# Optimization experiments

Measured on AMD Instinct MI355X. Metric: run time of the kernel, lower is better.

The kernel has to match this reference:

```python
import jax, jax.numpy as jnp
import numpy as np

N_NODES = 100000
N_EDGES = 1600000
IN_FEAT = 256
HIDDEN = 64
N_CLASSES = 16


def gcn_conv(x, edge_index, W, b):
    """PyG GCNConv: add self-loops, symmetric normalization, linear+aggregate."""
    n = x.shape[0]
    src, dst = edge_index[0], edge_index[1]
    loops = jnp.arange(n, dtype=src.dtype)
    src = jnp.concatenate([src, loops])
    dst = jnp.concatenate([dst, loops])
    # in-degree on graph with self-loops
    deg = jax.ops.segment_sum(jnp.ones(src.shape[0], dtype=x.dtype), dst, num_segments=n)
    dinv = jnp.where(deg > 0, jax.lax.rsqrt(deg), 0.0)
    h = x @ W                                  # [N, out]
    norm = dinv[src] * dinv[dst]               # [E+N]
    msg = h[src] * norm[:, None]                # gather + scale (memory-bound)
    out = jax.ops.segment_sum(msg, dst, num_segments=n)  # scatter-add
    return out + b


def setup_inputs() -> dict:
    key = jax.random.key(0)
    ks = jax.random.split(key, 5)
    x = jax.random.normal(ks[0], (N_NODES, IN_FEAT), dtype=jnp.float32)
    edge_index = jax.random.randint(ks[1], (2, N_EDGES), 0, N_NODES, dtype=jnp.int64)
    W1 = jax.random.normal(ks[2], (IN_FEAT, HIDDEN), dtype=jnp.float32) * (1.0 / np.sqrt(IN_FEAT))
    b1 = jnp.zeros((HIDDEN,), dtype=jnp.float32)
    W2 = jax.random.normal(ks[3], (HIDDEN, N_CLASSES), dtype=jnp.float32) * (1.0 / np.sqrt(HIDDEN))
    b2 = jnp.zeros((N_CLASSES,), dtype=jnp.float32)
    return {"x": x, "edge_index": edge_index, "W1": W1, "b1": b1, "W2": W2, "b2": b2}


def reference(x, edge_index, W1, b1, W2, b2):
    h = gcn_conv(x, edge_index, W1, b1)
    h = jax.nn.relu(h)
    # dropout p=0.5 is identity in eval mode (training=False)
    out = gcn_conv(h, edge_index, W2, b2)
    return out
```

## Files before the change

### kernel.cpp

```cpp
#include <hip/hip_runtime.h>

#define NN 100000
#define NE 1600000
#define FIN 256
#define FH 64
#define FC 16

#define SCAN_CHUNK 1024
#define NB_SCAN ((NN + SCAN_CHUNK - 1) / SCAN_CHUNK)
#define NB_COUNT ((NE + 255) / 256)
#define NB_GEMM1 ((NN + 63) / 64)
#define NB_FUSED (5 * NB_GEMM1)

typedef int v2i __attribute__((ext_vector_type(2)));

__device__ __forceinline__ float4 fma4(float4 v, float w, float4 a) {
    a.x = fmaf(v.x, w, a.x); a.y = fmaf(v.y, w, a.y);
    a.z = fmaf(v.z, w, a.z); a.w = fmaf(v.w, w, a.w);
    return a;
}
__device__ __forceinline__ float4 add4(float4 a, float4 v) {
    a.x += v.x; a.y += v.y; a.z += v.z; a.w += v.w;
    return a;
}
__device__ __forceinline__ float4 xor_add4(float4 r, int m) {
    r.x += __shfl_xor(r.x, m, 64); r.y += __shfl_xor(r.y, m, 64);
    r.z += __shfl_xor(r.z, m, 64); r.w += __shfl_xor(r.w, m, 64);
    return r;
}

__global__ void detect_k(const int* __restrict__ ei, int* __restrict__ flag) {
    if (threadIdx.x == 0 && blockIdx.x == 0) {
        int z = (ei[1] == 0) & (ei[3] == 0) & (ei[5] == 0) & (ei[7] == 0);
        *flag = z;
    }
}

__device__ __forceinline__ int eidx(const int* __restrict__ ei, int f, int pos) {
    return f ? ei[2 * pos] : ei[pos];
}

__global__ __launch_bounds__(256, 8) void fused_k(const int* __restrict__ ei,
                                                  const int* __restrict__ flag,
                                                  int* __restrict__ deg,
                                                  v2i* __restrict__ packed,
                                                  const float* __restrict__ x,
                                                  const float* __restrict__ W,
                                                  float* __restrict__ h) {
    __shared__ float As[32][68];
    __shared__ float Bs[32][64];
    const int b = blockIdx.x;
    if ((b % 5) != 4) {
        int cb = (b / 5) * 4 + (b % 5);
        if (cb >= NB_COUNT) return;
        int e = cb * 256 + threadIdx.x;
        if (e >= NE) return;
        int f = *flag;
        int s = eidx(ei, f, e);
        int d = eidx(ei, f, NE + e);
        int r = atomicAdd(&deg[d], 1);
        v2i p; p.x = s; p.y = d | (r << 17);
        packed[e] = p;
        return;
    }
    const int t = threadIdx.x;
    const int r0 = (b / 5) * 64;
    const int tx4 = (t & 15) * 4;
    const int ty4 = (t >> 4) * 4;
    const int xkf = (t & 7) * 4;
    const int xrow = t >> 3;
    const int wcol = (t & 15) * 4;
    const int wrow = t >> 4;

    float acc[4][4] = {};

    for (int k0 = 0; k0 < FIN; k0 += 32) {
        #pragma unroll
        for (int i = 0; i < 2; i++) {
            int row = xrow + 32 * i;
            int gr = r0 + row;
            float4 v = make_float4(0.f, 0.f, 0.f, 0.f);
            if (gr < NN) v = *(const float4*)&x[gr * FIN + k0 + xkf];
            As[xkf + 0][row] = v.x;
            As[xkf + 1][row] = v.y;
            As[xkf + 2][row] = v.z;
            As[xkf + 3][row] = v.w;
            int kr = wrow + 16 * i;
            float4 w = *(const float4*)&W[(k0 + kr) * FH + wcol];
            *(float4*)&Bs[kr][wcol] = w;
        }
        __syncthreads();
        #pragma unroll 8
        for (int kk = 0; kk < 32; kk++) {
            float4 a = *(const float4*)&As[kk][ty4];
            float4 bq = *(const float4*)&Bs[kk][tx4];
            float av[4] = {a.x, a.y, a.z, a.w};
            float bv[4] = {bq.x, bq.y, bq.z, bq.w};
            #pragma unroll
            for (int i2 = 0; i2 < 4; i2++)
                #pragma unroll
                for (int j2 = 0; j2 < 4; j2++)
                    acc[i2][j2] = fmaf(av[i2], bv[j2], acc[i2][j2]);
        }
        __syncthreads();
    }
    #pragma unroll
    for (int i2 = 0; i2 < 4; i2++) {
        int r = r0 + ty4 + i2;
        if (r < NN)
            *(float4*)&h[r * FH + tx4] =
                make_float4(acc[i2][0], acc[i2][1], acc[i2][2], acc[i2][3]);
    }
}

__global__ __launch_bounds__(256) void scan_sum_k(const int* __restrict__ deg,
                                                  int* __restrict__ partial,
                                                  float* __restrict__ dinv) {
    __shared__ int red[256];
    int b = blockIdx.x, t = threadIdx.x;
    int base = b * SCAN_CHUNK + t * 4;
    int s = 0;
    #pragma unroll
    for (int i = 0; i < 4; i++) {
        int idx = base + i;
        if (idx < NN) {
            int dv = deg[idx];
            s += dv;
            dinv[idx] = rsqrtf((float)(dv + 1));
        }
    }
    red[t] = s;
    __syncthreads();
    for (int off = 128; off > 0; off >>= 1) {
        if (t < off) red[t] += red[t + off];
        __syncthreads();
    }
    if (t == 0) partial[b] = red[0];
}

__global__ __launch_bounds__(256) void scale1_k(float* __restrict__ h1,
                                                const float* __restrict__ dinv) {
    int i = blockIdx.x * 256 + threadIdx.x;
    if (i >= NN * 16) return;
    int row = i >> 4;
    float d = dinv[row];
    float4 v = *(const float4*)&h1[i * 4];
    v.x *= d; v.y *= d; v.z *= d; v.w *= d;
    *(float4*)&h1[i * 4] = v;
}

__global__ __launch_bounds__(128) void scan_part_k(int* __restrict__ partial) {
    __shared__ int s[128];
    int t = threadIdx.x;
    int v = (t < NB_SCAN) ? partial[t] : 0;
    s[t] = v; __syncthreads();
    for (int off = 1; off < 128; off <<= 1) {
        int u = (t >= off) ? s[t - off] : 0;
        __syncthreads();
        s[t] += u;
        __syncthreads();
    }
    if (t < NB_SCAN) partial[t] = s[t] - v;
}

__global__ __launch_bounds__(256) void scan_out_k(const int* __restrict__ deg,
                                                  const int* __restrict__ partial,
                                                  int* __restrict__ row_start) {
    __shared__ int s[256];
    int b = blockIdx.x, t = threadIdx.x;
    int base = b * SCAN_CHUNK + t * 4;
    int v[4]; int sum = 0;
    #pragma unroll
    for (int i = 0; i < 4; i++) {
        int idx = base + i;
        v[i] = (idx < NN) ? deg[idx] : 0;
        sum += v[i];
    }
    s[t] = sum; __syncthreads();
    for (int off = 1; off < 256; off <<= 1) {
        int u = (t >= off) ? s[t - off] : 0;
        __syncthreads();
        s[t] += u;
        __syncthreads();
    }
    int run = partial[b] + s[t] - sum;
    #pragma unroll
    for (int i = 0; i < 4; i++) {
        int idx = base + i;
        if (idx < NN) {
            row_start[idx] = run;
            run += v[i];
            if (idx == NN - 1) row_start[NN] = run;
        }
    }
}

__global__ __launch_bounds__(256) void fill_k(const v2i* __restrict__ packed,
                                              const int* __restrict__ row_start,
                                              int* __restrict__ csr) {
    int e = blockIdx.x * 256 + threadIdx.x;
    if (e >= NE) return;
    v2i p = __builtin_nontemporal_load(&packed[e]);
    int d = p.y & 0x1FFFF;
    int r = ((unsigned)p.y) >> 17;
    csr[row_start[d] + r] = p.x;
}

__global__ __launch_bounds__(256) void agg1g_k(const int* __restrict__ csr,
                                               const int* __restrict__ row_start,
                                               const float* __restrict__ h1,
                                               const float* __restrict__ dinv,
                                               const float* __restrict__ b1,
                                               const float* __restrict__ W2,
                                               float* __restrict__ h2) {
    __shared__ float sW2[FH * FC];
    __shared__ float sp[4][FH];
    const int t = threadIdx.x;
    #pragma unroll
    for (int i = 0; i < 4; i++) sW2[t + 256 * i] = W2[t + 256 * i];
    __syncthreads();

    int wid = t >> 6;
    int n = blockIdx.x * 4 + wid;
    int lane = t & 63;
    if (n >= NN) return;
    int sg = lane >> 4;
    int fl = lane & 15;
    int s0 = row_start[n], s1 = row_start[n + 1];
    float4 A = make_float4(0.f, 0.f, 0.f, 0.f);
    float4 B = make_float4(0.f, 0.f, 0.f, 0.f);
    float4 C = make_float4(0.f, 0.f, 0.f, 0.f);
    float4 D = make_float4(0.f, 0.f, 0.f, 0.f);
    for (int j0 = s0; j0 < s1; j0 += 64) {
        int idx = j0 + lane;
        int sl = (idx < s1) ? csr[idx] : 0;
        int cnt = s1 - j0; if (cnt > 64) cnt = 64;
        int j = 0;
        for (; j + 16 <= cnt; j += 16) {
            int eA = __shfl(sl, j + sg, 64);
            int eB = __shfl(sl, j + 4 + sg, 64);
            int eC = __shfl(sl, j + 8 + sg, 64);
            int eD = __shfl(sl, j + 12 + sg, 64);
            float4 vA = *(const float4*)&h1[eA * FH + fl * 4];
            float4 vB = *(const float4*)&h1[eB * FH + fl * 4];
            float4 vC = *(const float4*)&h1[eC * FH + fl * 4];
            float4 vD = *(const float4*)&h1[eD * FH + fl * 4];
            A = add4(A, vA); B = add4(B, vB);
            C = add4(C, vC); D = add4(D, vD);
        }
        if (j + 8 <= cnt) {
            int eA = __shfl(sl, j + sg, 64);
            int eB = __shfl(sl, j + 4 + sg, 64);
            float4 vA = *(const float4*)&h1[eA * FH + fl * 4];
            float4 vB = *(const float4*)&h1[eB * FH + fl * 4];
            A = add4(A, vA); B = add4(B, vB);
            j += 8;
        }
        if (j + 4 <= cnt) {
            int eA = __shfl(sl, j + sg, 64);
            float4 vA = *(const float4*)&h1[eA * FH + fl * 4];
            A = add4(A, vA);
            j += 4;
        }
        int rem = cnt - j;
        if (rem > 0) {
            int jj = j + (sg < rem ? sg : 0);
            int eA = __shfl(sl, jj, 64);
            float wA = (sg < rem) ? 1.f : 0.f;
            float4 vA = *(const float4*)&h1[eA * FH + fl * 4];
            A = fma4(vA, wA, A);
        }
    }
    float4 r = add4(add4(A, B), add4(C, D));
    r = xor_add4(r, 16);
    r = xor_add4(r, 32);
    float dn = dinv[n];
    if (sg == 0) {
        float4 self = *(const float4*)&h1[n * FH + fl * 4];
        float4 bq = *(const float4*)&b1[fl * 4];
        float4 p;
        p.x = fmaxf(fmaf(r.x + self.x, dn, bq.x), 0.f);
        p.y = fmaxf(fmaf(r.y + self.y, dn, bq.y), 0.f);
        p.z = fmaxf(fmaf(r.z + self.z, dn, bq.z), 0.f);
        p.w = fmaxf(fmaf(r.w + self.w, dn, bq.w), 0.f);
        *(float4*)&sp[wid][fl * 4] = p;
    }
    __builtin_amdgcn_s_waitcnt(0);
    if (lane < FC) {
        float o = 0.f;
        #pragma unroll 8
        for (int k = 0; k < FH; k++)
            o = fmaf(sp[wid][k], sW2[k * FC + lane], o);
        h2[n * FC + lane] = o * dn;
    }
}

__global__ __launch_bounds__(256) void agg2_k(const int* __restrict__ csr,
                                              const int* __restrict__ row_start,
                                              const float* __restrict__ h2,
                                              const float* __restrict__ dinv,
                                              const float* __restrict__ b2,
                                              float* __restrict__ out) {
    const int t = threadIdx.x;
    int n = blockIdx.x * 16 + (t >> 4);
    int l16 = t & 15;
    int base = t & 48;
    int q = (t >> 2) & 3;
    int c = t & 3;
    if (n >= NN) return;
    int s0 = row_start[n], s1 = row_start[n + 1];
    float4 A = make_float4(0.f, 0.f, 0.f, 0.f);
    float4 B = make_float4(0.f, 0.f, 0.f, 0.f);
    float4 C = make_float4(0.f, 0.f, 0.f, 0.f);
    float4 D = make_float4(0.f, 0.f, 0.f, 0.f);
    for (int j0 = s0; j0 < s1; j0 += 16) {
        int idx = j0 + l16;
        int sl = (idx < s1) ? csr[idx] : 0;
        int cnt = s1 - j0; if (cnt > 16) cnt = 16;
        int j = 0;
        if (j + 16 <= cnt) {
            int eA = __shfl(sl, base + j + q, 64);
            int eB = __shfl(sl, base + j + 4 + q, 64);
            int eC = __shfl(sl, base + j + 8 + q, 64);
            int eD = __shfl(sl, base + j + 12 + q, 64);
            float4 vA = *(const float4*)&h2[eA * FC + c * 4];
            float4 vB = *(const float4*)&h2[eB * FC + c * 4];
            float4 vC = *(const float4*)&h2[eC * FC + c * 4];
            float4 vD = *(const float4*)&h2[eD * FC + c * 4];
            A = add4(A, vA); B = add4(B, vB);
            C = add4(C, vC); D = add4(D, vD);
            j += 16;
        }
        if (j + 8 <= cnt) {
            int eA = __shfl(sl, base + j + q, 64);
            int eB = __shfl(sl, base + j + 4 + q, 64);
            float4 vA = *(const float4*)&h2[eA * FC + c * 4];
            float4 vB = *(const float4*)&h2[eB * FC + c * 4];
            A = add4(A, vA); B = add4(B, vB);
            j += 8;
        }
        if (j + 4 <= cnt) {
            int eA = __shfl(sl, base + j + q, 64);
            float4 vA = *(const float4*)&h2[eA * FC + c * 4];
            A = add4(A, vA);
            j += 4;
        }
        int rem = cnt - j;
        if (rem > 0) {
            int jj = base + j + (q < rem ? q : 0);
            int eA = __shfl(sl, jj, 64);
            float wA = (q < rem) ? 1.f : 0.f;
            float4 vA = *(const float4*)&h2[eA * FC + c * 4];
            A = fma4(vA, wA, A);
        }
    }
    float4 r = add4(add4(A, B), add4(C, D));
    r = xor_add4(r, 4);
    r = xor_add4(r, 8);
    if (q == 0) {
        float dn = dinv[n];
        float4 self = *(const float4*)&h2[n * FC + c * 4];
        float4 bq = *(const float4*)&b2[c * 4];
        float4 p;
        p.x = fmaf(r.x + self.x, dn, bq.x);
        p.y = fmaf(r.y + self.y, dn, bq.y);
        p.z = fmaf(r.z + self.z, dn, bq.z);
        p.w = fmaf(r.w + self.w, dn, bq.w);
        *(float4*)&out[n * FC + c * 4] = p;
    }
}

extern "C" void kernel_launch(void* const* d_in, const int* in_sizes, int n_in,
                              void* d_out, int out_size, void* d_ws, size_t ws_size,
                              hipStream_t stream) {
    const float* x  = (const float*)d_in[0];
    const int*   ei = (const int*)d_in[1];
    const float* W1 = (const float*)d_in[2];
    const float* b1 = (const float*)d_in[3];
    const float* W2 = (const float*)d_in[4];
    const float* b2 = (const float*)d_in[5];
    float* out = (float*)d_out;

    char* ws = (char*)d_ws;
    int*   deg       = (int*)(ws + 0);
    int*   row_start = (int*)(ws + 512 * 1024);
    float* dinv      = (float*)(ws + 1024 * 1024);
    int*   flag      = (int*)(ws + 1536 * 1024);
    int*   partial   = (int*)(ws + 1540 * 1024);
    int*   csr       = (int*)(ws + 2ull * 1024 * 1024);
    float* h1        = (float*)(ws + 9ull * 1024 * 1024);
    v2i*   packed    = (v2i*)(ws + 35ull * 1024 * 1024);
    float* h2        = (float*)(ws + 35ull * 1024 * 1024);

    detect_k<<<1, 64, 0, stream>>>(ei, flag);
    (void)hipMemsetAsync(deg, 0, NN * sizeof(int), stream);
    fused_k<<<NB_FUSED, 256, 0, stream>>>(ei, flag, deg, packed, x, W1, h1);
    scan_sum_k<<<NB_SCAN, 256, 0, stream>>>(deg, partial, dinv);
    scale1_k<<<(NN * 16 + 255) / 256, 256, 0, stream>>>(h1, dinv);
    scan_part_k<<<1, 128, 0, stream>>>(partial);
    scan_out_k<<<NB_SCAN, 256, 0, stream>>>(deg, partial, row_start);
    fill_k<<<(NE + 255) / 256, 256, 0, stream>>>(packed, row_start, csr);

    agg1g_k<<<(NN + 3) / 4, 256, 0, stream>>>(csr, row_start, h1, dinv, b1, W2, h2);
    agg2_k<<<(NN + 15) / 16, 256, 0, stream>>>(csr, row_start, h2, dinv, b2, out);
}
```

Baseline: 361.7 us.

## Compute first GEMM with split-bf16 MFMA instead of FP32 shared-memory tiling

Replaces the FP32 LDS-tiled x@W1 GEMM with MFMA bf16 instructions that use a hi/lo split (three products) to approximate FP32 accuracy. A small prep kernel pre-splits W1 into bf16 hi/lo fragments in MFMA layout and also takes over the edge-format detection. The GEMM tile grows to 128 rows per block and the interleaved degree-count blocks change to an 8:1 ratio. The x loads go straight from global memory without LDS, and the output stores become scalar, which may hurt coalescing.

Result: faster. 353.9 us (-2.1%).

```diff
diff --git a/kernel.cpp b/kernel.cpp
--- a/kernel.cpp
+++ b/kernel.cpp
@@ -9,10 +9,12 @@
 #define SCAN_CHUNK 1024
 #define NB_SCAN ((NN + SCAN_CHUNK - 1) / SCAN_CHUNK)
 #define NB_COUNT ((NE + 255) / 256)
-#define NB_GEMM1 ((NN + 63) / 64)
-#define NB_FUSED (5 * NB_GEMM1)
+#define NB_GEMM1 ((NN + 127) / 128)
+#define NB_FUSED (9 * NB_GEMM1)
 
 typedef int v2i __attribute__((ext_vector_type(2)));
+typedef short s16x8 __attribute__((ext_vector_type(8)));
+typedef float f32x4 __attribute__((ext_vector_type(4)));
 
 __device__ __forceinline__ float4 fma4(float4 v, float w, float4 a) {
     a.x = fmaf(v.x, w, a.x); a.y = fmaf(v.y, w, a.y);
@@ -29,10 +31,21 @@
     return r;
 }
 
-__global__ void detect_k(const int* __restrict__ ei, int* __restrict__ flag) {
-    if (threadIdx.x == 0 && blockIdx.x == 0) {
-        int z = (ei[1] == 0) & (ei[3] == 0) & (ei[5] == 0) & (ei[7] == 0);
-        *flag = z;
+__device__ __forceinline__ unsigned short bf16rne(float f) {
+    unsigned u = __float_as_uint(f);
+    u += 0x7FFFu + ((u >> 16) & 1u);
+    return (unsigned short)(u >> 16);
+}
+
+__device__ __forceinline__ void split8(const float* f, s16x8& hi, s16x8& lo) {
+    #pragma unroll
+    for (int i = 0; i < 8; i++) {
+        unsigned u = __float_as_uint(f[i]);
+        unsigned short h = (unsigned short)((u + 0x7FFFu + ((u >> 16) & 1u)) >> 16);
+        float l = f[i] - __uint_as_float((unsigned)h << 16);
+        unsigned ul = __float_as_uint(l);
+        hi[i] = (short)h;
+        lo[i] = (short)((ul + 0x7FFFu + ((ul >> 16) & 1u)) >> 16);
     }
 }
 
@@ -40,18 +53,46 @@
     return f ? ei[2 * pos] : ei[pos];
 }
 
-__global__ __launch_bounds__(256, 8) void fused_k(const int* __restrict__ ei,
+__global__ __launch_bounds__(256) void prep_k(const int* __restrict__ ei,
+                                              int* __restrict__ flag,
+                                              const float* __restrict__ W,
+                                              unsigned short* __restrict__ Whi,
+                                              unsigned short* __restrict__ Wlo) {
+    int b = blockIdx.x;
+    if (b == 8) {
+        if (threadIdx.x == 0) {
+            int z = (ei[1] == 0) & (ei[3] == 0) & (ei[5] == 0) & (ei[7] == 0);
+            *flag = z;
+        }
+        return;
+    }
+    int slot = b * 256 + threadIdx.x;
+    int l = slot & 63;
+    int c = (slot >> 6) & 3;
+    int s = slot >> 8;
+    int k0 = s * 32 + (l >> 4) * 8;
+    int col = c * 16 + (l & 15);
+    #pragma unroll
+    for (int i = 0; i < 8; i++) {
+        float f = W[(k0 + i) * FH + col];
+        unsigned short h = bf16rne(f);
+        float lres = f - __uint_as_float((unsigned)h << 16);
+        Whi[slot * 8 + i] = h;
+        Wlo[slot * 8 + i] = bf16rne(lres);
+    }
+}
+
+__global__ __launch_bounds__(256, 4) void fused_k(const int* __restrict__ ei,
                                                   const int* __restrict__ flag,
                                                   int* __restrict__ deg,
                                                   v2i* __restrict__ packed,
                                                   const float* __restrict__ x,
-                                                  const float* __restrict__ W,
-                                                  float* __restrict__ h) {
-    __shared__ float As[32][68];
-    __shared__ float Bs[32][64];
+                                                  const unsigned short* __restrict__ Whi,
+                                                  const unsigned short* __restrict__ Wlo,
+                                                  float* __restrict__ h1) {
     const int b = blockIdx.x;
-    if ((b % 5) != 4) {
-        int cb = (b / 5) * 4 + (b % 5);
+    if ((b % 9) != 8) {
+        int cb = (b / 9) * 8 + (b % 9);
         if (cb >= NB_COUNT) return;
         int e = cb * 256 + threadIdx.x;
         if (e >= NE) return;
@@ -64,52 +105,59 @@
         return;
     }
     const int t = threadIdx.x;
-    const int r0 = (b / 5) * 64;
-    const int tx4 = (t & 15) * 4;
-    const int ty4 = (t >> 4) * 4;
-    const int xkf = (t & 7) * 4;
-    const int xrow = t >> 3;
-    const int wcol = (t & 15) * 4;
-    const int wrow = t >> 4;
-
-    float acc[4][4] = {};
-
-    for (int k0 = 0; k0 < FIN; k0 += 32) {
+    const int lane = t & 63;
+    const int wid = t >> 6;
+    const int mb = (b / 9) * 128 + wid * 32;
+    const int lr = lane & 15;
+    const int lk = (lane >> 4) * 8;
+
+    int ra0 = mb + lr;
+    int ra1 = mb + 16 + lr;
+    const float* pa0 = x + (size_t)(ra0 < NN ? ra0 : NN - 1) * FIN + lk;
+    const float* pa1 = x + (size_t)(ra1 < NN ? ra1 : NN - 1) * FIN + lk;
+
+    f32x4 acc[2][4] = {};
+
+    for (int s = 0; s < 8; s++) {
+        float fa0[8], fa1[8];
+        float4 q;
+        q = *(const float4*)(pa0 + s * 32);
+        fa0[0] = q.x; fa0[1] = q.y; fa0[2] = q.z; fa0[3] = q.w;
+        q = *(const float4*)(pa0 + s * 32 + 4);
+        fa0[4] = q.x; fa0[5] = q.y; fa0[6] = q.z; fa0[7] = q.w;
+        q = *(const float4*)(pa1 + s * 32);
+        fa1[0] = q.x; fa1[1] = q.y; fa1[2] = q.z; fa1[3] = q.w;
+        q = *(const float4*)(pa1 + s * 32 + 4);
+        fa1[4] = q.x; fa1[5] = q.y; fa1[6] = q.z; fa1[7] = q.w;
+
+        s16x8 a0h, a0l, a1h, a1l;
+        split8(fa0, a0h, a0l);
+        split8(fa1, a1h, a1l);
+
         #pragma unroll
-        for (int i = 0; i < 2; i++) {
-            int row = xrow + 32 * i;
-            int gr = r0 + row;
-            float4 v = make_float4(0.f, 0.f, 0.f, 0.f);
-            if (gr < NN) v = *(const float4*)&x[gr * FIN + k0 + xkf];
-            As[xkf + 0][row] = v.x;
-            As[xkf + 1][row] = v.y;
-            As[xkf + 2][row] = v.z;
-            As[xkf + 3][row] = v.w;
-            int kr = wrow + 16 * i;
-            float4 w = *(const float4*)&W[(k0 + kr) * FH + wcol];
-            *(float4*)&Bs[kr][wcol] = w;
-        }
-        __syncthreads();
-        #pragma unroll 8
-        for (int kk = 0; kk < 32; kk++) {
-            float4 a = *(const float4*)&As[kk][ty4];
-            float4 bq = *(const float4*)&Bs[kk][tx4];
-            float av[4] = {a.x, a.y, a.z, a.w};
-            float bv[4] = {bq.x, bq.y, bq.z, bq.w};
+        for (int c = 0; c < 4; c++) {
+            s16x8 wh = *(const s16x8*)&Whi[((s * 4 + c) * 64 + lane) * 8];
+            s16x8 wl = *(const s16x8*)&Wlo[((s * 4 + c) * 64 + lane) * 8];
+            acc[0][c] = __builtin_amdgcn_mfma_f32_16x16x32_bf16(a0h, wh, acc[0][c], 0, 0, 0);
+            acc[0][c] = __builtin_amdgcn_mfma_f32_16x16x32_bf16(a0l, wh, acc[0][c], 0, 0, 0);
+            acc[0][c] = __builtin_amdgcn_mfma_f32_16x16x32_bf16(a0h, wl, acc[0][c], 0, 0, 0);
+            acc[1][c] = __builtin_amdgcn_mfma_f32_16x16x32_bf16(a1h, wh, acc[1][c], 0, 0, 0);
+            acc[1][c] = __builtin_amdgcn_mfma_f32_16x16x32_bf16(a1l, wh, acc[1][c], 0, 0, 0);
+            acc[1][c] = __builtin_amdgcn_mfma_f32_16x16x32_bf16(a1h, wl, acc[1][c], 0, 0, 0);
+        }
+    }
+    #pragma unroll
+    for (int r = 0; r < 2; r++) {
+        int rowb = mb + 16 * r + (lane >> 4) * 4;
+        #pragma unroll
+        for (int c = 0; c < 4; c++) {
             #pragma unroll
-            for (int i2 = 0; i2 < 4; i2++)
-                #pragma unroll
-                for (int j2 = 0; j2 < 4; j2++)
-                    acc[i2][j2] = fmaf(av[i2], bv[j2], acc[i2][j2]);
-        }
-        __syncthreads();
-    }
-    #pragma unroll
-    for (int i2 = 0; i2 < 4; i2++) {
-        int r = r0 + ty4 + i2;
-        if (r < NN)
-            *(float4*)&h[r * FH + tx4] =
-                make_float4(acc[i2][0], acc[i2][1], acc[i2][2], acc[i2][3]);
+            for (int v = 0; v < 4; v++) {
+                int row = rowb + v;
+                if (row < NN)
+                    h1[(size_t)row * FH + 16 * c + lr] = acc[r][c][v];
+            }
+        }
     }
 }
 
@@ -387,14 +435,16 @@
     float* dinv      = (float*)(ws + 1024 * 1024);
     int*   flag      = (int*)(ws + 1536 * 1024);
     int*   partial   = (int*)(ws + 1540 * 1024);
+    unsigned short* Whi = (unsigned short*)(ws + 1544 * 1024);
+    unsigned short* Wlo = (unsigned short*)(ws + 1584 * 1024);
     int*   csr       = (int*)(ws + 2ull * 1024 * 1024);
     float* h1        = (float*)(ws + 9ull * 1024 * 1024);
     v2i*   packed    = (v2i*)(ws + 35ull * 1024 * 1024);
     float* h2        = (float*)(ws + 35ull * 1024 * 1024);
 
-    detect_k<<<1, 64, 0, stream>>>(ei, flag);
+    prep_k<<<9, 256, 0, stream>>>(ei, flag, W1, Whi, Wlo);
     (void)hipMemsetAsync(deg, 0, NN * sizeof(int), stream);
-    fused_k<<<NB_FUSED, 256, 0, stream>>>(ei, flag, deg, packed, x, W1, h1);
+    fused_k<<<NB_FUSED, 256, 0, stream>>>(ei, flag, deg, packed, x, Whi, Wlo, h1);
     scan_sum_k<<<NB_SCAN, 256, 0, stream>>>(deg, partial, dinv);
     scale1_k<<<(NN * 16 + 255) / 256, 256, 0, stream>>>(h1, dinv);
     scan_part_k<<<1, 128, 0, stream>>>(partial);
```
